# Optimization experiments

Measured on AMD Instinct MI355X. Metric: run time of the kernel, lower is better.

## Reference

```python
import jax, jax.numpy as jnp
import numpy as np

G, D, H, O = 8, 1024, 2048, 1024

def _xavier(key, shape):
    # xavier_normal_ on nn.Linear weight [out, in]: std = sqrt(2/(fan_in+fan_out))
    fan_out, fan_in = shape[-2], shape[-1]
    std = float(np.sqrt(2.0 / (fan_in + fan_out)))
    return jax.random.normal(key, shape, dtype=jnp.float32) * std

def setup_inputs() -> dict:
    key = jax.random.key(0)
    kx, kg, ku, kd = jax.random.split(key, 4)
    x = jax.random.normal(kx, (65536, D), dtype=jnp.float32)
    # weights stored per-group in nn.Linear layout [out, in]
    Wg = _xavier(kg, (G, H, D))
    Wu = _xavier(ku, (G, H, D))
    Wd = _xavier(kd, (G, O, H))
    return {"x": x, "Wg": Wg, "Wu": Wu, "Wd": Wd}

def reference(x, Wg, Wu, Wd):
    # x: [B*G, D] -> [B, G, D]
    xb = x.reshape(-1, G, D)
    gate = jnp.einsum('bgd,ghd->bgh', xb, Wg)   # [B, G, H]
    up = jnp.einsum('bgd,ghd->bgh', xb, Wu)     # [B, G, H]
    hidden = jax.nn.silu(gate) * up             # fused SwiGLU
    out = jnp.einsum('bgh,goh->bgo', hidden, Wd)  # [B, G, O]
    return out.reshape(-1, O)
```

## Files before the change

### kernel.cpp

```cpp
#include <hip/hip_runtime.h>


#define GN 8
#define DN 1024
#define HN 2048
#define ON 1024

typedef __attribute__((ext_vector_type(8))) short short8;
typedef __attribute__((ext_vector_type(4))) float f32x4;
typedef __attribute__((ext_vector_type(4))) unsigned int u32x4;

#define SBAR() __builtin_amdgcn_sched_barrier(0)
#define BARR() __builtin_amdgcn_s_barrier()
#define WAIT_LGKM0()                                       \
  do {                                                     \
    asm volatile("s_waitcnt lgkmcnt(0)" ::: "memory");     \
    __builtin_amdgcn_sched_barrier(0);                     \
  } while (0)

#define DS128(dst, base, imm)                                                  \
  asm volatile("ds_read_b128 %0, %1 offset:" #imm                              \
               : "=v"(dst)                                                     \
               : "v"((const __attribute__((address_space(3))) unsigned short*)(base)))

__device__ __forceinline__ void async16(const void* g, void* l) {
  __builtin_amdgcn_global_load_lds(
      (const __attribute__((address_space(1))) void*)g,
      (__attribute__((address_space(3))) void*)l, 16, 0, 0);
}

__device__ __forceinline__ unsigned short f2bf(float f) {
  unsigned int u = __float_as_uint(f);
  u += 0x7FFFu + ((u >> 16) & 1u);
  return (unsigned short)(u >> 16);
}

__global__ __launch_bounds__(256) void cvt_f32_bf16(
    const float* __restrict__ in, unsigned short* __restrict__ out, int n) {
  int t = blockIdx.x * 256 + threadIdx.x;
  int i = t * 8;
  if (i >= n) return;
  f32x4 a = *(const f32x4*)(in + i);
  f32x4 b = *(const f32x4*)(in + i + 4);
  u32x4 r;
  r.x = (unsigned)f2bf(a.x) | ((unsigned)f2bf(a.y) << 16);
  r.y = (unsigned)f2bf(a.z) | ((unsigned)f2bf(a.w) << 16);
  r.z = (unsigned)f2bf(b.x) | ((unsigned)f2bf(b.y) << 16);
  r.w = (unsigned)f2bf(b.z) | ((unsigned)f2bf(b.w) << 16);
  *(u32x4*)(out + i) = r;
}

__global__ __launch_bounds__(512, 2) void gemm1_swiglu(
    const unsigned short* __restrict__ Xb, const unsigned short* __restrict__ Wgb,
    const unsigned short* __restrict__ Wub, unsigned short* __restrict__ Hid) {
  extern __shared__ unsigned short sm[];
  unsigned short* sA = sm;
  unsigned short* sG = sm + 32768;
  unsigned short* sU = sm + 49152;

  const int bid = blockIdx.x;
  const int swz = (bid & 7) * 512 + (bid >> 3);
  const int g = swz >> 9;
  const int rem = swz & 511;
  const int m0 = (rem >> 4) * 256;
  const int n0 = (rem & 15) * 128;

  const int tid = threadIdx.x;
  const int lane = tid & 63;
  const int w = tid >> 6;
  const int wm = w >> 2, wn = w & 3;
  const int fr = lane & 15, fc = lane >> 4;
  const int sR = (fc + ((fr >> 1) & 3)) & 3;

  const unsigned short* aSrc[2];
  unsigned short* aDst[2];
#pragma unroll
  for (int j = 0; j < 2; ++j) {
    int R = j * 128 + w * 16 + (lane >> 2);
    int c = ((lane & 3) - ((R >> 1) & 3)) & 3;
    aSrc[j] = Xb + ((size_t)((m0 + R) * 8 + g)) * DN + c * 8;
    aDst[j] = &sA[(j * 128 + w * 16) * 32];
  }
  const unsigned short *gSrc, *uSrc;
  unsigned short *gDst, *uDst;
  {
    int R = w * 16 + (lane >> 2);
    int c = ((lane & 3) - ((R >> 1) & 3)) & 3;
    gSrc = Wgb + ((size_t)(g * HN + n0 + R)) * DN + c * 8;
    uSrc = Wub + ((size_t)(g * HN + n0 + R)) * DN + c * 8;
    gDst = &sG[(w * 16) * 32];
    uDst = &sU[(w * 16) * 32];
  }

  auto stageA = [&](int t, int kk) {
    const int buf = (t & 1) * 2 + kk;
    const int ko = t * 64 + kk * 32;
#pragma unroll
    for (int j = 0; j < 2; ++j) async16(aSrc[j] + ko, aDst[j] + buf * 8192);
  };
  auto stageB = [&](int t, int kk) {
    const int buf = (t & 1) * 2 + kk;
    const int ko = t * 64 + kk * 32;
    async16(gSrc + ko, gDst + buf * 4096);
    async16(uSrc + ko, uDst + buf * 4096);
  };
  auto readA = [&](int t, int kk, short8* a) {
    const unsigned short* p =
        sA + ((t & 1) * 2 + kk) * 8192 + (wm * 128 + fr) * 32 + sR * 8;
    DS128(a[0], p, 0);
    DS128(a[1], p, 1024);
    DS128(a[2], p, 2048);
    DS128(a[3], p, 3072);
    DS128(a[4], p, 4096);
    DS128(a[5], p, 5120);
    DS128(a[6], p, 6144);
    DS128(a[7], p, 7168);
  };
  auto readB = [&](const unsigned short* base, int t, int kk, short8* b) {
    const unsigned short* p =
        base + ((t & 1) * 2 + kk) * 4096 + (wn * 32 + fr) * 32 + sR * 8;
    DS128(b[0], p, 0);
    DS128(b[1], p, 1024);
  };

  f32x4 accg[8][2], accu[8][2];
#pragma unroll
  for (int mi = 0; mi < 8; ++mi)
#pragma unroll
    for (int ni = 0; ni < 2; ++ni) {
      accg[mi][ni] = (f32x4)(0.0f);
      accu[mi][ni] = (f32x4)(0.0f);
    }

  auto mm16 = [&](const short8* a, const short8* b, f32x4(*acc)[2]) {
    __builtin_amdgcn_s_setprio(1);
#pragma unroll
    for (int mi = 0; mi < 8; ++mi)
#pragma unroll
      for (int ni = 0; ni < 2; ++ni)
        acc[mi][ni] = __builtin_amdgcn_mfma_f32_16x16x32_bf16(
            a[mi], b[ni], acc[mi][ni], 0, 0, 0);
    __builtin_amdgcn_s_setprio(0);
  };

  stageA(0, 0); stageB(0, 0); stageA(0, 1); stageB(0, 1);
  stageA(1, 0); stageB(1, 0); stageA(1, 1);
  asm volatile("s_waitcnt vmcnt(6)" ::: "memory");
  BARR();

  short8 af[8], bg[2], bu[2];
  const int NIT = DN / 128;
#pragma unroll 1
  for (int i = 0; i < NIT; ++i) {
    const int T = 2 * i;
    const bool full = (i + 1 < NIT);
    readA(T, 0, af); readB(sG, T, 0, bg);
    stageB(T + 1, 1);
    BARR();
    WAIT_LGKM0();
    mm16(af, bg, accg);
    BARR();
    readB(sU, T, 0, bu);
    if (full) stageA(T + 2, 0);
    BARR();
    WAIT_LGKM0();
    mm16(af, bu, accu);
    BARR();
    readA(T, 1, af); readB(sG, T, 1, bg);
    if (full) stageB(T + 2, 0);
    BARR();
    WAIT_LGKM0();
    mm16(af, bg, accg);
    BARR();
    readB(sU, T, 1, bu);
    if (full) stageA(T + 2, 1);
    BARR();
    WAIT_LGKM0();
    mm16(af, bu, accu);
    if (full) { asm volatile("s_waitcnt vmcnt(6)" ::: "memory"); }
    else      { asm volatile("s_waitcnt vmcnt(0)" ::: "memory"); }
    BARR();
    readA(T + 1, 0, af); readB(sG, T + 1, 0, bg);
    if (full) stageB(T + 2, 1);
    BARR();
    WAIT_LGKM0();
    mm16(af, bg, accg);
    BARR();
    readB(sU, T + 1, 0, bu);
    if (full) stageA(T + 3, 0);
    BARR();
    WAIT_LGKM0();
    mm16(af, bu, accu);
    BARR();
    readA(T + 1, 1, af); readB(sG, T + 1, 1, bg);
    if (full) stageB(T + 3, 0);
    BARR();
    WAIT_LGKM0();
    mm16(af, bg, accg);
    BARR();
    readB(sU, T + 1, 1, bu);
    if (full) stageA(T + 3, 1);
    BARR();
    WAIT_LGKM0();
    mm16(af, bu, accu);
    if (full) { asm volatile("s_waitcnt vmcnt(6)" ::: "memory"); }
    BARR();
  }

  const int q = lane >> 4, cl = lane & 15;
#pragma unroll
  for (int mi = 0; mi < 8; ++mi)
#pragma unroll
    for (int ni = 0; ni < 2; ++ni) {
      int hcol = n0 + wn * 32 + ni * 16 + cl;
#pragma unroll
      for (int i2 = 0; i2 < 4; ++i2) {
        int b = m0 + wm * 128 + mi * 16 + q * 4 + i2;
        float gf = accg[mi][ni][i2];
        float uf = accu[mi][ni][i2];
        float hv = (gf / (1.0f + __expf(-gf))) * uf;
        Hid[((size_t)(b * 8 + g)) * HN + hcol] = f2bf(hv);
      }
    }
}

__global__ __launch_bounds__(512, 2) void gemm2_down(
    const unsigned short* __restrict__ Hid, const unsigned short* __restrict__ Wdb,
    float* __restrict__ Out) {
  extern __shared__ unsigned short sm[];
  unsigned short* sA = sm;
  unsigned short* sB = sm + 32768;

  const int bid = blockIdx.x;
  const int swz = (bid & 7) * 128 + (bid >> 3);
  const int g = swz >> 7;
  const int rem = swz & 127;
  const int m0 = (rem >> 2) * 256;
  const int n0 = (rem & 3) * 256;

  const int tid = threadIdx.x;
  const int lane = tid & 63;
  const int w = tid >> 6;
  const int wm = w >> 2, wn = w & 3;
  const int fr = lane & 15, fc = lane >> 4;
  const int sR = (fc + ((fr >> 1) & 3)) & 3;

  const unsigned short* aSrc[2];
  const unsigned short* bSrc[2];
  unsigned short* aDst[2];
  unsigned short* bDst[2];
#pragma unroll
  for (int j = 0; j < 2; ++j) {
    int R = j * 128 + w * 16 + (lane >> 2);
    int c = ((lane & 3) - ((R >> 1) & 3)) & 3;
    aSrc[j] = Hid + ((size_t)((m0 + R) * 8 + g)) * HN + c * 8;
    bSrc[j] = Wdb + ((size_t)(g * ON + n0 + R)) * HN + c * 8;
    aDst[j] = &sA[(j * 128 + w * 16) * 32];
    bDst[j] = &sB[(j * 128 + w * 16) * 32];
  }

  auto stageA = [&](int t, int kk) {
    const int buf = (t & 1) * 2 + kk;
    const int ko = t * 64 + kk * 32;
#pragma unroll
    for (int j = 0; j < 2; ++j) async16(aSrc[j] + ko, aDst[j] + buf * 8192);
  };
  auto stageB = [&](int t, int kk) {
    const int buf = (t & 1) * 2 + kk;
    const int ko = t * 64 + kk * 32;
#pragma unroll
    for (int j = 0; j < 2; ++j) async16(bSrc[j] + ko, bDst[j] + buf * 8192);
  };
  auto readA = [&](int t, int kk, short8* a) {
    const unsigned short* p =
        sA + ((t & 1) * 2 + kk) * 8192 + (wm * 128 + fr) * 32 + sR * 8;
    DS128(a[0], p, 0);
    DS128(a[1], p, 1024);
    DS128(a[2], p, 2048);
    DS128(a[3], p, 3072);
    DS128(a[4], p, 4096);
    DS128(a[5], p, 5120);
    DS128(a[6], p, 6144);
    DS128(a[7], p, 7168);
  };
  auto readB = [&](int t, int kk, int nb, short8* b) {
    const unsigned short* p =
        sB + ((t & 1) * 2 + kk) * 8192 + (wn * 64 + nb * 16 + fr) * 32 + sR * 8;
    DS128(b[0], p, 0);
    DS128(b[1], p, 1024);
  };

  f32x4 acc[8][4];
#pragma unroll
  for (int mi = 0; mi < 8; ++mi)
#pragma unroll
    for (int ni = 0; ni < 4; ++ni) acc[mi][ni] = (f32x4)(0.0f);

  auto mm16 = [&](const short8* a, const short8* b, int nb) {
    __builtin_amdgcn_s_setprio(1);
#pragma unroll
    for (int mi = 0; mi < 8; ++mi)
#pragma unroll
      for (int nj = 0; nj < 2; ++nj)
        acc[mi][nb + nj] = __builtin_amdgcn_mfma_f32_16x16x32_bf16(
            a[mi], b[nj], acc[mi][nb + nj], 0, 0, 0);
    __builtin_amdgcn_s_setprio(0);
  };

  stageA(0, 0); stageB(0, 0); stageA(0, 1); stageB(0, 1);
  stageA(1, 0); stageB(1, 0); stageA(1, 1);
  asm volatile("s_waitcnt vmcnt(6)" ::: "memory");
  BARR();

  short8 af[8], bf[2];
  const int NIT = HN / 128;
#pragma unroll 1
  for (int i = 0; i < NIT; ++i) {
    const int T = 2 * i;
    const bool full = (i + 1 < NIT);
    readA(T, 0, af); readB(T, 0, 0, bf);
    stageB(T + 1, 1);
    BARR();
    WAIT_LGKM0();
    mm16(af, bf, 0);
    BARR();
    readB(T, 0, 2, bf);
    if (full) stageA(T + 2, 0);
    BARR();
    WAIT_LGKM0();
    mm16(af, bf, 2);
    BARR();
    readA(T, 1, af); readB(T, 1, 0, bf);
    if (full) stageB(T + 2, 0);
    BARR();
    WAIT_LGKM0();
    mm16(af, bf, 0);
    BARR();
    readB(T, 1, 2, bf);
    if (full) stageA(T + 2, 1);
    BARR();
    WAIT_LGKM0();
    mm16(af, bf, 2);
    if (full) { asm volatile("s_waitcnt vmcnt(6)" ::: "memory"); }
    else      { asm volatile("s_waitcnt vmcnt(0)" ::: "memory"); }
    BARR();
    readA(T + 1, 0, af); readB(T + 1, 0, 0, bf);
    if (full) stageB(T + 2, 1);
    BARR();
    WAIT_LGKM0();
    mm16(af, bf, 0);
    BARR();
    readB(T + 1, 0, 2, bf);
    if (full) stageA(T + 3, 0);
    BARR();
    WAIT_LGKM0();
    mm16(af, bf, 2);
    BARR();
    readA(T + 1, 1, af); readB(T + 1, 1, 0, bf);
    if (full) stageB(T + 3, 0);
    BARR();
    WAIT_LGKM0();
    mm16(af, bf, 0);
    BARR();
    readB(T + 1, 1, 2, bf);
    if (full) stageA(T + 3, 1);
    BARR();
    WAIT_LGKM0();
    mm16(af, bf, 2);
    if (full) { asm volatile("s_waitcnt vmcnt(6)" ::: "memory"); }
    BARR();
  }

  const int q = lane >> 4, cl = lane & 15;
#pragma unroll
  for (int mi = 0; mi < 8; ++mi)
#pragma unroll
    for (int ni = 0; ni < 4; ++ni) {
      int o = n0 + wn * 64 + ni * 16 + cl;
#pragma unroll
      for (int i2 = 0; i2 < 4; ++i2) {
        int b = m0 + wm * 128 + mi * 16 + q * 4 + i2;
        Out[((size_t)(b * 8 + g)) * ON + o] = acc[mi][ni][i2];
      }
    }
}

extern "C" void kernel_launch(void* const* d_in, const int* in_sizes, int n_in,
                              void* d_out, int out_size, void* d_ws, size_t ws_size,
                              hipStream_t stream) {
  const float* x  = (const float*)d_in[0];
  const float* Wg = (const float*)d_in[1];
  const float* Wu = (const float*)d_in[2];
  const float* Wd = (const float*)d_in[3];
  float* out = (float*)d_out;

  const int NX = 65536 * 1024;
  const int NW = GN * HN * DN;

  unsigned short* xb = (unsigned short*)d_ws;
  unsigned short* wg = xb + (size_t)NX;
  unsigned short* wu = wg + (size_t)NW;
  unsigned short* wd = wu + (size_t)NW;
  unsigned short* hid = wd + (size_t)NW;

  static bool once = false;
  if (!once) {
    hipFuncSetAttribute((const void*)gemm1_swiglu,
                        hipFuncAttributeMaxDynamicSharedMemorySize, 131072);
    hipFuncSetAttribute((const void*)gemm2_down,
                        hipFuncAttributeMaxDynamicSharedMemorySize, 131072);
    once = true;
  }

  cvt_f32_bf16<<<NX / 8 / 256, 256, 0, stream>>>(x, xb, NX);
  cvt_f32_bf16<<<NW / 8 / 256, 256, 0, stream>>>(Wg, wg, NW);
  cvt_f32_bf16<<<NW / 8 / 256, 256, 0, stream>>>(Wu, wu, NW);
  cvt_f32_bf16<<<NW / 8 / 256, 256, 0, stream>>>(Wd, wd, NW);

  gemm1_swiglu<<<dim3(4096), dim3(512), 131072, stream>>>(xb, wg, wu, hid);
  gemm2_down<<<dim3(1024), dim3(512), 131072, stream>>>(hid, wd, out);
}
```

Before: 1.355 ms.

## Make both GEMMs persistent with 256 blocks looping over M tiles

Both GEMM kernels now launch 256 persistent blocks (one per CU) instead of 4096/1024 blocks. Each block walks several consecutive M tiles for a fixed (group, N-tile), and the async-load pipeline continues across tile boundaries. The epilogue (SwiGLU or the fp32 store) runs inside the loop every 16 or 32 K-steps and then resets the accumulators. This removes per-block prologue and pipeline-fill costs and keeps the weight tile warm. In exchange the epilogue stores now stall the pipeline, the grid is hardcoded to 256 CUs, and the occupancy hint of 2 blocks per CU can no longer be used.

After: 1.356 ms. Within noise of the previous version (+0.1%).

```diff
diff --git a/kernel.cpp b/kernel.cpp
--- a/kernel.cpp
+++ b/kernel.cpp
@@ -10,7 +10,6 @@
 typedef __attribute__((ext_vector_type(4))) float f32x4;
 typedef __attribute__((ext_vector_type(4))) unsigned int u32x4;
 
-#define SBAR() __builtin_amdgcn_sched_barrier(0)
 #define BARR() __builtin_amdgcn_s_barrier()
 #define WAIT_LGKM0()                                       \
   do {                                                     \
@@ -59,11 +58,9 @@
   unsigned short* sU = sm + 49152;
 
   const int bid = blockIdx.x;
-  const int swz = (bid & 7) * 512 + (bid >> 3);
-  const int g = swz >> 9;
-  const int rem = swz & 511;
-  const int m0 = (rem >> 4) * 256;
-  const int n0 = (rem & 15) * 128;
+  const int g = bid >> 5;
+  const int n0 = ((bid >> 1) & 15) * 128;
+  const int mh = bid & 1;
 
   const int tid = threadIdx.x;
   const int lane = tid & 63;
@@ -72,13 +69,13 @@
   const int fr = lane & 15, fc = lane >> 4;
   const int sR = (fc + ((fr >> 1) & 3)) & 3;
 
-  const unsigned short* aSrc[2];
+  const unsigned short* aBase[2];
   unsigned short* aDst[2];
 #pragma unroll
   for (int j = 0; j < 2; ++j) {
     int R = j * 128 + w * 16 + (lane >> 2);
     int c = ((lane & 3) - ((R >> 1) & 3)) & 3;
-    aSrc[j] = Xb + ((size_t)((m0 + R) * 8 + g)) * DN + c * 8;
+    aBase[j] = Xb + ((size_t)((mh * 4096 + R) * 8 + g)) * DN + c * 8;
     aDst[j] = &sA[(j * 128 + w * 16) * 32];
   }
   const unsigned short *gSrc, *uSrc;
@@ -92,21 +89,23 @@
     uDst = &sU[(w * 16) * 32];
   }
 
-  auto stageA = [&](int t, int kk) {
-    const int buf = (t & 1) * 2 + kk;
-    const int ko = t * 64 + kk * 32;
-#pragma unroll
-    for (int j = 0; j < 2; ++j) async16(aSrc[j] + ko, aDst[j] + buf * 8192);
-  };
-  auto stageB = [&](int t, int kk) {
-    const int buf = (t & 1) * 2 + kk;
-    const int ko = t * 64 + kk * 32;
+  auto stageA = [&](int Tg, int kk) {
+    const int buf = (Tg & 1) * 2 + kk;
+    const size_t toff = (size_t)(Tg >> 4) * (256u * 8u * DN);
+    const int ko = (Tg & 15) * 64 + kk * 32;
+#pragma unroll
+    for (int j = 0; j < 2; ++j)
+      async16(aBase[j] + toff + ko, aDst[j] + buf * 8192);
+  };
+  auto stageB = [&](int Tg, int kk) {
+    const int buf = (Tg & 1) * 2 + kk;
+    const int ko = (Tg & 15) * 64 + kk * 32;
     async16(gSrc + ko, gDst + buf * 4096);
     async16(uSrc + ko, uDst + buf * 4096);
   };
-  auto readA = [&](int t, int kk, short8* a) {
+  auto readA = [&](int Tg, int kk, short8* a) {
     const unsigned short* p =
-        sA + ((t & 1) * 2 + kk) * 8192 + (wm * 128 + fr) * 32 + sR * 8;
+        sA + ((Tg & 1) * 2 + kk) * 8192 + (wm * 128 + fr) * 32 + sR * 8;
     DS128(a[0], p, 0);
     DS128(a[1], p, 1024);
     DS128(a[2], p, 2048);
@@ -116,9 +115,9 @@
     DS128(a[6], p, 6144);
     DS128(a[7], p, 7168);
   };
-  auto readB = [&](const unsigned short* base, int t, int kk, short8* b) {
+  auto readB = [&](const unsigned short* base, int Tg, int kk, short8* b) {
     const unsigned short* p =
-        base + ((t & 1) * 2 + kk) * 4096 + (wn * 32 + fr) * 32 + sR * 8;
+        base + ((Tg & 1) * 2 + kk) * 4096 + (wn * 32 + fr) * 32 + sR * 8;
     DS128(b[0], p, 0);
     DS128(b[1], p, 1024);
   };
@@ -149,11 +148,12 @@
   BARR();
 
   short8 af[8], bg[2], bu[2];
-  const int NIT = DN / 128;
+  const int q = lane >> 4, cl = lane & 15;
+  const int NIT = 128;
 #pragma unroll 1
-  for (int i = 0; i < NIT; ++i) {
-    const int T = 2 * i;
-    const bool full = (i + 1 < NIT);
+  for (int it = 0; it < NIT; ++it) {
+    const int T = 2 * it;
+    const bool full = (it + 1 < NIT);
     readA(T, 0, af); readB(sG, T, 0, bg);
     stageB(T + 1, 1);
     BARR();
@@ -205,23 +205,27 @@
     mm16(af, bu, accu);
     if (full) { asm volatile("s_waitcnt vmcnt(6)" ::: "memory"); }
     BARR();
-  }
-
-  const int q = lane >> 4, cl = lane & 15;
-#pragma unroll
-  for (int mi = 0; mi < 8; ++mi)
-#pragma unroll
-    for (int ni = 0; ni < 2; ++ni) {
-      int hcol = n0 + wn * 32 + ni * 16 + cl;
-#pragma unroll
-      for (int i2 = 0; i2 < 4; ++i2) {
-        int b = m0 + wm * 128 + mi * 16 + q * 4 + i2;
-        float gf = accg[mi][ni][i2];
-        float uf = accu[mi][ni][i2];
-        float hv = (gf / (1.0f + __expf(-gf))) * uf;
-        Hid[((size_t)(b * 8 + g)) * HN + hcol] = f2bf(hv);
-      }
+    if ((T & 15) == 14) {
+      const int tile = T >> 4;
+      const int m0 = (mh * 16 + tile) * 256;
+#pragma unroll
+      for (int mi = 0; mi < 8; ++mi)
+#pragma unroll
+        for (int ni = 0; ni < 2; ++ni) {
+          int hcol = n0 + wn * 32 + ni * 16 + cl;
+#pragma unroll
+          for (int i2 = 0; i2 < 4; ++i2) {
+            int b = m0 + wm * 128 + mi * 16 + q * 4 + i2;
+            float gf = accg[mi][ni][i2];
+            float uf = accu[mi][ni][i2];
+            float hv = (gf / (1.0f + __expf(-gf))) * uf;
+            Hid[((size_t)(b * 8 + g)) * HN + hcol] = f2bf(hv);
+          }
+          accg[mi][ni] = (f32x4)(0.0f);
+          accu[mi][ni] = (f32x4)(0.0f);
+        }
     }
+  }
 }
 
 __global__ __launch_bounds__(512, 2) void gemm2_down(
@@ -232,11 +236,9 @@
   unsigned short* sB = sm + 32768;
 
   const int bid = blockIdx.x;
-  const int swz = (bid & 7) * 128 + (bid >> 3);
-  const int g = swz >> 7;
-  const int rem = swz & 127;
-  const int m0 = (rem >> 2) * 256;
-  const int n0 = (rem & 3) * 256;
+  const int g = bid >> 5;
+  const int n0 = ((bid >> 3) & 3) * 256;
+  const int mq = bid & 7;
 
   const int tid = threadIdx.x;
   const int lane = tid & 63;
@@ -245,7 +247,7 @@
   const int fr = lane & 15, fc = lane >> 4;
   const int sR = (fc + ((fr >> 1) & 3)) & 3;
 
-  const unsigned short* aSrc[2];
+  const unsigned short* aBase[2];
   const unsigned short* bSrc[2];
   unsigned short* aDst[2];
   unsigned short* bDst[2];
@@ -253,27 +255,29 @@
   for (int j = 0; j < 2; ++j) {
     int R = j * 128 + w * 16 + (lane >> 2);
     int c = ((lane & 3) - ((R >> 1) & 3)) & 3;
-    aSrc[j] = Hid + ((size_t)((m0 + R) * 8 + g)) * HN + c * 8;
+    aBase[j] = Hid + ((size_t)((mq * 1024 + R) * 8 + g)) * HN + c * 8;
     bSrc[j] = Wdb + ((size_t)(g * ON + n0 + R)) * HN + c * 8;
     aDst[j] = &sA[(j * 128 + w * 16) * 32];
     bDst[j] = &sB[(j * 128 + w * 16) * 32];
   }
 
-  auto stageA = [&](int t, int kk) {
-    const int buf = (t & 1) * 2 + kk;
-    const int ko = t * 64 + kk * 32;
-#pragma unroll
-    for (int j = 0; j < 2; ++j) async16(aSrc[j] + ko, aDst[j] + buf * 8192);
-  };
-  auto stageB = [&](int t, int kk) {
-    const int buf = (t & 1) * 2 + kk;
-    const int ko = t * 64 + kk * 32;
+  auto stageA = [&](int Tg, int kk) {
+    const int buf = (Tg & 1) * 2 + kk;
+    const size_t toff = (size_t)(Tg >> 5) * (256u * 8u * HN);
+    const int ko = (Tg & 31) * 64 + kk * 32;
+#pragma unroll
+    for (int j = 0; j < 2; ++j)
+      async16(aBase[j] + toff + ko, aDst[j] + buf * 8192);
+  };
+  auto stageB = [&](int Tg, int kk) {
+    const int buf = (Tg & 1) * 2 + kk;
+    const int ko = (Tg & 31) * 64 + kk * 32;
 #pragma unroll
     for (int j = 0; j < 2; ++j) async16(bSrc[j] + ko, bDst[j] + buf * 8192);
   };
-  auto readA = [&](int t, int kk, short8* a) {
+  auto readA = [&](int Tg, int kk, short8* a) {
     const unsigned short* p =
-        sA + ((t & 1) * 2 + kk) * 8192 + (wm * 128 + fr) * 32 + sR * 8;
+        sA + ((Tg & 1) * 2 + kk) * 8192 + (wm * 128 + fr) * 32 + sR * 8;
     DS128(a[0], p, 0);
     DS128(a[1], p, 1024);
     DS128(a[2], p, 2048);
@@ -283,9 +287,9 @@
     DS128(a[6], p, 6144);
     DS128(a[7], p, 7168);
   };
-  auto readB = [&](int t, int kk, int nb, short8* b) {
+  auto readB = [&](int Tg, int kk, int nb, short8* b) {
     const unsigned short* p =
-        sB + ((t & 1) * 2 + kk) * 8192 + (wn * 64 + nb * 16 + fr) * 32 + sR * 8;
+        sB + ((Tg & 1) * 2 + kk) * 8192 + (wn * 64 + nb * 16 + fr) * 32 + sR * 8;
     DS128(b[0], p, 0);
     DS128(b[1], p, 1024);
   };
@@ -313,11 +317,12 @@
   BARR();
 
   short8 af[8], bf[2];
-  const int NIT = HN / 128;
+  const int q = lane >> 4, cl = lane & 15;
+  const int NIT = 64;
 #pragma unroll 1
-  for (int i = 0; i < NIT; ++i) {
-    const int T = 2 * i;
-    const bool full = (i + 1 < NIT);
+  for (int it = 0; it < NIT; ++it) {
+    const int T = 2 * it;
+    const bool full = (it + 1 < NIT);
     readA(T, 0, af); readB(T, 0, 0, bf);
     stageB(T + 1, 1);
     BARR();
@@ -369,20 +374,23 @@
     mm16(af, bf, 2);
     if (full) { asm volatile("s_waitcnt vmcnt(6)" ::: "memory"); }
     BARR();
-  }
-
-  const int q = lane >> 4, cl = lane & 15;
-#pragma unroll
-  for (int mi = 0; mi < 8; ++mi)
-#pragma unroll
-    for (int ni = 0; ni < 4; ++ni) {
-      int o = n0 + wn * 64 + ni * 16 + cl;
-#pragma unroll
-      for (int i2 = 0; i2 < 4; ++i2) {
-        int b = m0 + wm * 128 + mi * 16 + q * 4 + i2;
-        Out[((size_t)(b * 8 + g)) * ON + o] = acc[mi][ni][i2];
-      }
+    if ((T & 31) == 30) {
+      const int tile = T >> 5;
+      const int m0 = (mq * 4 + tile) * 256;
+#pragma unroll
+      for (int mi = 0; mi < 8; ++mi)
+#pragma unroll
+        for (int ni = 0; ni < 4; ++ni) {
+          int o = n0 + wn * 64 + ni * 16 + cl;
+#pragma unroll
+          for (int i2 = 0; i2 < 4; ++i2) {
+            int b = m0 + wm * 128 + mi * 16 + q * 4 + i2;
+            Out[((size_t)(b * 8 + g)) * ON + o] = acc[mi][ni][i2];
+          }
+          acc[mi][ni] = (f32x4)(0.0f);
+        }
     }
+  }
 }
 
 extern "C" void kernel_launch(void* const* d_in, const int* in_sizes, int n_in,
@@ -417,6 +425,6 @@
   cvt_f32_bf16<<<NW / 8 / 256, 256, 0, stream>>>(Wu, wu, NW);
   cvt_f32_bf16<<<NW / 8 / 256, 256, 0, stream>>>(Wd, wd, NW);
 
-  gemm1_swiglu<<<dim3(4096), dim3(512), 131072, stream>>>(xb, wg, wu, hid);
-  gemm2_down<<<dim3(1024), dim3(512), 131072, stream>>>(hid, wd, out);
-}
+  gemm1_swiglu<<<dim3(256), dim3(512), 131072, stream>>>(xb, wg, wu, hid);
+  gemm2_down<<<dim3(256), dim3(512), 131072, stream>>>(hid, wd, out);
+}
```
